# Kernel tuning notes

Measured on AMD Instinct MI355X. Metric: run time of the kernel, lower is better.

Reference implementation:

```python
import jax, jax.numpy as jnp
import numpy as np

N_MESS = 50000
MAX_NEI = 8
INPUT_SIZE = 128
H_SIZE = 128
DEPTH = 5


def setup_inputs() -> dict:
    key = jax.random.key(0)
    ks = jax.random.split(key, 7)
    s = 0.05
    fmess = jax.random.normal(ks[0], (N_MESS, INPUT_SIZE), dtype=jnp.float32)
    bgraph = jax.random.randint(ks[1], (N_MESS, MAX_NEI), 0, N_MESS, dtype=jnp.int32)
    # torch nn.Linear weights are [out_features, in_features]
    W_z = jax.random.normal(ks[2], (H_SIZE, INPUT_SIZE + H_SIZE), dtype=jnp.float32) * s
    b_z = jnp.zeros((H_SIZE,), jnp.float32)
    W_r = jax.random.normal(ks[3], (H_SIZE, INPUT_SIZE), dtype=jnp.float32) * s  # no bias
    U_r = jax.random.normal(ks[4], (H_SIZE, H_SIZE), dtype=jnp.float32) * s
    b_Ur = jnp.zeros((H_SIZE,), jnp.float32)
    W_h = jax.random.normal(ks[5], (H_SIZE, INPUT_SIZE + H_SIZE), dtype=jnp.float32) * s
    b_h = jnp.zeros((H_SIZE,), jnp.float32)
    return {"fmess": fmess, "bgraph": bgraph, "W_z": W_z, "b_z": b_z,
            "W_r": W_r, "U_r": U_r, "b_Ur": b_Ur, "W_h": W_h, "b_h": b_h}


def _gru_step(fmess, h_nei, W_z, b_z, W_r, U_r, b_Ur, W_h, b_h):
    # h_nei: [N, K, H]
    sum_h = h_nei.sum(axis=1)                                     # [N, H]
    z = jax.nn.sigmoid(jnp.concatenate([fmess, sum_h], axis=1) @ W_z.T + b_z)
    r_1 = (fmess @ W_r.T)[:, None, :]                             # [N, 1, H]
    r_2 = jnp.einsum('nkh,gh->nkg', h_nei, U_r) + b_Ur            # [N, K, H]
    r = jax.nn.sigmoid(r_1 + r_2)
    sum_gated_h = (r * h_nei).sum(axis=1)                         # [N, H]
    pre_h = jnp.tanh(jnp.concatenate([fmess, sum_gated_h], axis=1) @ W_h.T + b_h)
    return (1.0 - z) * sum_h + z * pre_h


def reference(fmess, bgraph, W_z, b_z, W_r, U_r, b_Ur, W_h, b_h):
    n = fmess.shape[0]
    h = jnp.zeros((n, H_SIZE), dtype=fmess.dtype)
    mask = jnp.ones((n, 1), dtype=fmess.dtype).at[0, 0].set(0.0)  # message 0 is padding
    for _ in range(DEPTH):
        h_nei = h[bgraph]                                         # gather: [N, K, H]
        h = _gru_step(fmess, h_nei, W_z, b_z, W_r, U_r, b_Ur, W_h, b_h)
        h = h * mask
    return h
```

## Files before the change

### kernel.cpp

```cpp
#include <hip/hip_runtime.h>
#include <hip/hip_bf16.h>

#define NM 50000
#define HD 128
#define KNEI 8
#define BM 64
#define SPAD 136
#define NBLK ((NM + BM - 1) / BM)
#define NH ((size_t)NM * (size_t)HD)

typedef float  fx4   __attribute__((ext_vector_type(4)));
typedef short  s16x8 __attribute__((ext_vector_type(8)));
typedef short  s16x4 __attribute__((ext_vector_type(4)));

__device__ __forceinline__ float sigm_f(float x) {
    return __builtin_amdgcn_rcpf(1.0f + __expf(-x));
}
__device__ __forceinline__ float tanh_f(float x) {
    return 2.0f * sigm_f(2.0f * x) - 1.0f;
}
__device__ __forceinline__ unsigned short f2b(float f) {
    __hip_bfloat16 h = __float2bfloat16(f);
    return __builtin_bit_cast(unsigned short, h);
}
__device__ __forceinline__ float b2f(unsigned short u) {
    __hip_bfloat16 h = __builtin_bit_cast(__hip_bfloat16, u);
    return __bfloat162float(h);
}

#define MFMA16(a, b, c) __builtin_amdgcn_mfma_f32_16x16x32_bf16(a, b, c, 0, 0, 0)

__device__ __forceinline__ void load_bfrag(const unsigned short* __restrict__ W,
                                           int ldw, int woff, int nf0, int l,
                                           s16x8 (&bf)[2][4])
{
    #pragma unroll
    for (int j = 0; j < 2; ++j) {
        const unsigned short* p =
            W + (size_t)((nf0 + j) * 16 + (l & 15)) * ldw + woff + ((l >> 4) << 3);
        #pragma unroll
        for (int ks = 0; ks < 4; ++ks)
            bf[j][ks] = *(const s16x8*)(p + ks * 32);
    }
}

__device__ __forceinline__ void pass(const unsigned short (*As)[SPAD],
                                     const s16x8 (&bf)[2][4],
                                     int l, fx4 (&acc)[4][2])
{
    const int kq = (l >> 4) << 3;
    #pragma unroll
    for (int ks = 0; ks < 4; ++ks)
        #pragma unroll
        for (int rb = 0; rb < 4; ++rb) {
            const s16x8 a = *(const s16x8*)&As[rb * 16 + (l & 15)][ks * 32 + kq];
            acc[rb][0] = MFMA16(a, bf[0][ks], acc[rb][0]);
            acc[rb][1] = MFMA16(a, bf[1][ks], acc[rb][1]);
        }
}

#define ZACC2(acc) { _Pragma("unroll") for (int z_ = 0; z_ < 4; ++z_) { \
                     acc[z_][0] = (fx4)0.0f; acc[z_][1] = (fx4)0.0f; } }

__device__ __forceinline__ void stage_A32(const float* __restrict__ A, int row0,
                                          unsigned short (*As)[SPAD], int tid)
{
    const int r  = tid & 63;
    const int c0 = (tid >> 6) << 5;
    int gr = row0 + r; if (gr >= NM) gr = NM - 1;
    const float* ap = A + (size_t)gr * HD + c0;
    #pragma unroll
    for (int j = 0; j < 32; j += 8) {
        s16x8 s;
        #pragma unroll
        for (int q = 0; q < 8; ++q) s[q] = (short)f2b(ap[j + q]);
        *(s16x8*)&As[r][c0 + j] = s;
    }
}

__device__ __forceinline__ void stage_A16(const unsigned short* __restrict__ A16, int row0,
                                          unsigned short (*As)[SPAD], int tid)
{
    const int r  = tid & 63;
    const int c0 = (tid >> 6) << 5;
    int gr = row0 + r; if (gr >= NM) gr = NM - 1;
    const unsigned short* ap = A16 + (size_t)gr * HD + c0;
    #pragma unroll
    for (int j = 0; j < 32; j += 8)
        *(s16x8*)&As[r][c0 + j] = *(const s16x8*)(ap + j);
}

__device__ __forceinline__ void lds_to_g16(const unsigned short (*L)[SPAD], int row0,
                                           unsigned short* __restrict__ G, int tid)
{
    const int r  = tid & 63;
    const int c0 = (tid >> 6) << 5;
    const int gr = row0 + r;
    if (gr >= NM) return;
    #pragma unroll
    for (int j = 0; j < 32; j += 8)
        *(s16x8*)&G[(size_t)gr * HD + c0 + j] = *(const s16x8*)&L[r][c0 + j];
}

__global__ __launch_bounds__(256)
void dgru_wcvt(const float* __restrict__ Wz, const float* __restrict__ Wr,
               const float* __restrict__ Ur, const float* __restrict__ Wh,
               unsigned short* __restrict__ w16)
{
    const int i = blockIdx.x * 256 + threadIdx.x;
    float v;
    if      (i < 32768) v = Wz[i];
    else if (i < 49152) v = Wr[i - 32768];
    else if (i < 65536) v = Ur[i - 49152];
    else                v = Wh[i - 65536];
    w16[i] = f2b(v);
}

__global__ __launch_bounds__(256, 3)
void dgru_pre(const float* __restrict__ fmess,
              const unsigned short* __restrict__ wz16,
              const unsigned short* __restrict__ wr16,
              const unsigned short* __restrict__ wh16,
              const unsigned short* __restrict__ ur16,
              const float* __restrict__ bz, const float* __restrict__ bh,
              const float* __restrict__ bur,
              unsigned short* __restrict__ fmess16,
              unsigned short* __restrict__ pre_r16,
              unsigned short* __restrict__ h16, unsigned short* __restrict__ uh16)
{
    __shared__ unsigned short AsF[BM][SPAD];
    __shared__ unsigned short AsX[BM][SPAD];
    const int tid  = threadIdx.x;
    const int row0 = blockIdx.x * BM;
    const int l    = tid & 63;
    const int nf0  = (tid >> 6) << 1;
    const int col0 = nf0 * 16 + (l & 15);
    const int rq   = (l >> 4) << 2;

    s16x8 bfA[2][4], bfB[2][4];
    load_bfrag(wz16, 2 * HD, 0, nf0, l, bfA);
    load_bfrag(wr16, HD, 0, nf0, l, bfB);
    stage_A32(fmess, row0, AsF, tid);
    __syncthreads();

    lds_to_g16(AsF, row0, fmess16, tid);

    fx4 zacc[4][2]; ZACC2(zacc);
    pass(AsF, bfA, l, zacc);
    load_bfrag(wh16, 2 * HD, 0, nf0, l, bfA);
    {
        fx4 racc[4][2]; ZACC2(racc);
        pass(AsF, bfB, l, racc);
        #pragma unroll
        for (int rb = 0; rb < 4; ++rb)
            #pragma unroll
            for (int j = 0; j < 2; ++j)
                #pragma unroll
                for (int q = 0; q < 4; ++q)
                    AsX[rb * 16 + rq + q][col0 + j * 16] = f2b(racc[rb][j][q]);
    }
    __syncthreads();
    lds_to_g16(AsX, row0, pre_r16, tid);

    fx4 hacc[4][2]; ZACC2(hacc);
    pass(AsF, bfA, l, hacc);
    load_bfrag(ur16, HD, 0, nf0, l, bfB);
    #pragma unroll
    for (int rb = 0; rb < 4; ++rb)
        #pragma unroll
        for (int j = 0; j < 2; ++j) {
            const float bvz = bz[col0 + j * 16];
            const float bvh = bh[col0 + j * 16];
            #pragma unroll
            for (int q = 0; q < 4; ++q) {
                const int gr = row0 + rb * 16 + rq + q;
                float h0 = sigm_f(zacc[rb][j][q] + bvz) * tanh_f(hacc[rb][j][q] + bvh);
                if (gr == 0) h0 = 0.0f;
                hacc[rb][j][q] = h0;
            }
        }
    __syncthreads();
    #pragma unroll
    for (int rb = 0; rb < 4; ++rb)
        #pragma unroll
        for (int j = 0; j < 2; ++j)
            #pragma unroll
            for (int q = 0; q < 4; ++q)
                AsX[rb * 16 + rq + q][col0 + j * 16] = f2b(hacc[rb][j][q]);
    __syncthreads();
    lds_to_g16(AsX, row0, h16, tid);
    {
        fx4 uacc[4][2]; ZACC2(uacc);
        pass(AsX, bfB, l, uacc);
        #pragma unroll
        for (int rb = 0; rb < 4; ++rb)
            #pragma unroll
            for (int j = 0; j < 2; ++j) {
                const float bv = bur[col0 + j * 16];
                #pragma unroll
                for (int q = 0; q < 4; ++q)
                    AsF[rb * 16 + rq + q][col0 + j * 16] = f2b(uacc[rb][j][q] + bv);
            }
    }
    __syncthreads();
    lds_to_g16(AsF, row0, uh16, tid);
}

__global__ __launch_bounds__(256)
void dgru_gather(const unsigned short* __restrict__ h16,
                 const unsigned short* __restrict__ uh16,
                 const int* __restrict__ bgraph,
                 const unsigned short* __restrict__ pre_r16,
                 unsigned short* __restrict__ sh16, unsigned short* __restrict__ sg16)
{
    const int tid = threadIdx.x;
    const int n   = blockIdx.x * 8 + (tid >> 5);
    const int d0  = (tid & 31) << 2;

    const int4* bg = (const int4*)(bgraph + (size_t)n * KNEI);
    const int4 b0 = bg[0], b1 = bg[1];
    const int idx[KNEI] = {b0.x, b0.y, b0.z, b0.w, b1.x, b1.y, b1.z, b1.w};

    s16x4 hr[KNEI], ur[KNEI];
    #pragma unroll
    for (int k = 0; k < KNEI; ++k)
        hr[k] = *(const s16x4*)&h16[(size_t)idx[k] * HD + d0];
    #pragma unroll
    for (int k = 0; k < KNEI; ++k)
        ur[k] = *(const s16x4*)&uh16[(size_t)idx[k] * HD + d0];
    const s16x4 prb = *(const s16x4*)&pre_r16[(size_t)n * HD + d0];
    float pr[4];
    #pragma unroll
    for (int j = 0; j < 4; ++j) pr[j] = b2f((unsigned short)prb[j]);

    float sh[4] = {0.f, 0.f, 0.f, 0.f};
    float sg[4] = {0.f, 0.f, 0.f, 0.f};
    #pragma unroll
    for (int k = 0; k < KNEI; ++k) {
        #pragma unroll
        for (int j = 0; j < 4; ++j) {
            const float hv = b2f((unsigned short)hr[k][j]);
            const float uv = b2f((unsigned short)ur[k][j]);
            sh[j] += hv;
            sg[j] = fmaf(sigm_f(pr[j] + uv), hv, sg[j]);
        }
    }
    s16x4 osh, osg;
    #pragma unroll
    for (int j = 0; j < 4; ++j) {
        osh[j] = (short)f2b(sh[j]);
        osg[j] = (short)f2b(sg[j]);
    }
    const size_t o = (size_t)n * HD + d0;
    *(s16x4*)&sh16[o] = osh;
    *(s16x4*)&sg16[o] = osg;
}

__global__ __launch_bounds__(256, 3)
void dgru_zh(const unsigned short* __restrict__ fmess16,
             const unsigned short* __restrict__ sh16,
             const unsigned short* __restrict__ sg16,
             const unsigned short* __restrict__ wz16,
             const unsigned short* __restrict__ wh16,
             const unsigned short* __restrict__ ur16,
             const float* __restrict__ bz, const float* __restrict__ bh,
             const float* __restrict__ bur,
             unsigned short* __restrict__ h16, unsigned short* __restrict__ uh16,
             float* __restrict__ hout, int last)
{
    __shared__ unsigned short AsF[BM][SPAD];
    __shared__ unsigned short AsX[BM][SPAD];
    const int tid  = threadIdx.x;
    const int row0 = blockIdx.x * BM;
    const int l    = tid & 63;
    const int nf0  = (tid >> 6) << 1;
    const int col0 = nf0 * 16 + (l & 15);
    const int rq   = (l >> 4) << 2;

    s16x8 bfA[2][4], bfB[2][4];
    load_bfrag(wz16, 2 * HD, 0,  nf0, l, bfA);
    load_bfrag(wz16, 2 * HD, HD, nf0, l, bfB);
    stage_A16(fmess16, row0, AsF, tid);
    stage_A16(sh16,    row0, AsX, tid);
    __syncthreads();

    fx4 zacc[4][2]; ZACC2(zacc);
    pass(AsF, bfA, l, zacc);
    pass(AsX, bfB, l, zacc);
    s16x4 shp[4][2];
    #pragma unroll
    for (int rb = 0; rb < 4; ++rb)
        #pragma unroll
        for (int j = 0; j < 2; ++j) {
            const float bv = bz[col0 + j * 16];
            #pragma unroll
            for (int q = 0; q < 4; ++q) {
                shp[rb][j][q] = (short)AsX[rb * 16 + rq + q][col0 + j * 16];
                zacc[rb][j][q] = sigm_f(zacc[rb][j][q] + bv);
            }
        }
    load_bfrag(wh16, 2 * HD, 0,  nf0, l, bfA);
    load_bfrag(wh16, 2 * HD, HD, nf0, l, bfB);
    __syncthreads();
    stage_A16(sg16, row0, AsX, tid);
    __syncthreads();

    fx4 hacc[4][2]; ZACC2(hacc);
    pass(AsF, bfA, l, hacc);
    pass(AsX, bfB, l, hacc);
    #pragma unroll
    for (int rb = 0; rb < 4; ++rb)
        #pragma unroll
        for (int j = 0; j < 2; ++j) {
            const float bv = bh[col0 + j * 16];
            #pragma unroll
            for (int q = 0; q < 4; ++q) {
                const int gr = row0 + rb * 16 + rq + q;
                const float zz = zacc[rb][j][q];
                const float sv = b2f((unsigned short)shp[rb][j][q]);
                float o = (1.0f - zz) * sv + zz * tanh_f(hacc[rb][j][q] + bv);
                if (gr == 0) o = 0.0f;
                hacc[rb][j][q] = o;
            }
        }
    if (last) {
        #pragma unroll
        for (int rb = 0; rb < 4; ++rb)
            #pragma unroll
            for (int j = 0; j < 2; ++j)
                #pragma unroll
                for (int q = 0; q < 4; ++q) {
                    const int gr = row0 + rb * 16 + rq + q;
                    if (gr < NM) hout[(size_t)gr * HD + col0 + j * 16] = hacc[rb][j][q];
                }
        return;
    }
    load_bfrag(ur16, HD, 0, nf0, l, bfA);
    __syncthreads();
    #pragma unroll
    for (int rb = 0; rb < 4; ++rb)
        #pragma unroll
        for (int j = 0; j < 2; ++j)
            #pragma unroll
            for (int q = 0; q < 4; ++q)
                AsF[rb * 16 + rq + q][col0 + j * 16] = f2b(hacc[rb][j][q]);
    __syncthreads();
    lds_to_g16(AsF, row0, h16, tid);
    {
        fx4 uacc[4][2]; ZACC2(uacc);
        pass(AsF, bfA, l, uacc);
        #pragma unroll
        for (int rb = 0; rb < 4; ++rb)
            #pragma unroll
            for (int j = 0; j < 2; ++j) {
                const float bv = bur[col0 + j * 16];
                #pragma unroll
                for (int q = 0; q < 4; ++q)
                    AsX[rb * 16 + rq + q][col0 + j * 16] = f2b(uacc[rb][j][q] + bv);
            }
    }
    __syncthreads();
    lds_to_g16(AsX, row0, uh16, tid);
}

extern "C" void kernel_launch(void* const* d_in, const int* in_sizes, int n_in,
                              void* d_out, int out_size, void* d_ws, size_t ws_size,
                              hipStream_t stream) {
    const float* fmess  = (const float*)d_in[0];
    const int*   bgraph = (const int*)  d_in[1];
    const float* W_z    = (const float*)d_in[2];
    const float* b_z    = (const float*)d_in[3];
    const float* W_r    = (const float*)d_in[4];
    const float* U_r    = (const float*)d_in[5];
    const float* b_Ur   = (const float*)d_in[6];
    const float* W_h    = (const float*)d_in[7];
    const float* b_h    = (const float*)d_in[8];

    unsigned short* ws16 = (unsigned short*)d_ws;
    unsigned short* fmess16 = ws16;
    unsigned short* pre_r16 = ws16 + NH;
    unsigned short* h16     = ws16 + 2 * NH;
    unsigned short* uh16    = ws16 + 3 * NH;
    unsigned short* sh16    = ws16 + 4 * NH;
    unsigned short* sg16    = ws16 + 5 * NH;
    unsigned short* w16     = ws16 + 6 * NH;
    unsigned short* wz16 = w16;
    unsigned short* wr16 = w16 + 32768;
    unsigned short* ur16 = w16 + 49152;
    unsigned short* wh16 = w16 + 65536;
    float* hout = (float*)d_out;

    dgru_wcvt<<<dim3(384), dim3(256), 0, stream>>>(W_z, W_r, U_r, W_h, w16);

    dgru_pre<<<dim3(NBLK), dim3(256), 0, stream>>>(
        fmess, wz16, wr16, wh16, ur16, b_z, b_h, b_Ur,
        fmess16, pre_r16, h16, uh16);

    for (int it = 1; it < 5; ++it) {
        dgru_gather<<<dim3(NM / 8), dim3(256), 0, stream>>>(
            h16, uh16, bgraph, pre_r16, sh16, sg16);
        dgru_zh<<<dim3(NBLK), dim3(256), 0, stream>>>(
            fmess16, sh16, sg16, wz16, wh16, ur16, b_z, b_h, b_Ur,
            h16, uh16, hout, (it == 4) ? 1 : 0);
    }
}
```

Before: 336.4 us.

## Fuse neighbor gather into GRU matmul kernel with ping-pong h buffers

Merges the separate gather kernel into the z/h GEMM kernel, so neighbor sums (sum_h and the gated sum) are built directly in shared memory rather than written to and reread from global memory. Because a block now reads neighbor rows that other blocks are updating, h and U_r·h are double-buffered across iterations. Blocks grow to 512 threads, one wave per 16-column slice, which halves the B-fragment registers per wave. This removes four kernel launches and the sh/sg round trips, at the cost of more per-block gather latency sitting in front of the MFMA work.

```diff
diff --git a/kernel.cpp b/kernel.cpp
--- a/kernel.cpp
+++ b/kernel.cpp
@@ -30,6 +30,29 @@
 
 #define MFMA16(a, b, c) __builtin_amdgcn_mfma_f32_16x16x32_bf16(a, b, c, 0, 0, 0)
 
+__device__ __forceinline__ void ldb1(const unsigned short* __restrict__ W,
+                                     int ldw, int woff, int w, int l, s16x8 (&bf)[4])
+{
+    const unsigned short* p =
+        W + (size_t)(w * 16 + (l & 15)) * ldw + woff + ((l >> 4) << 3);
+    #pragma unroll
+    for (int ks = 0; ks < 4; ++ks)
+        bf[ks] = *(const s16x8*)(p + ks * 32);
+}
+
+__device__ __forceinline__ void pass1(const unsigned short (*As)[SPAD],
+                                      const s16x8 (&bf)[4], int l, fx4 (&acc)[4])
+{
+    const int kq = (l >> 4) << 3;
+    #pragma unroll
+    for (int ks = 0; ks < 4; ++ks)
+        #pragma unroll
+        for (int rb = 0; rb < 4; ++rb) {
+            const s16x8 a = *(const s16x8*)&As[rb * 16 + (l & 15)][ks * 32 + kq];
+            acc[rb] = MFMA16(a, bf[ks], acc[rb]);
+        }
+}
+
 __device__ __forceinline__ void load_bfrag(const unsigned short* __restrict__ W,
                                            int ldw, int woff, int nf0, int l,
                                            s16x8 (&bf)[2][4])
@@ -78,18 +101,6 @@
     }
 }
 
-__device__ __forceinline__ void stage_A16(const unsigned short* __restrict__ A16, int row0,
-                                          unsigned short (*As)[SPAD], int tid)
-{
-    const int r  = tid & 63;
-    const int c0 = (tid >> 6) << 5;
-    int gr = row0 + r; if (gr >= NM) gr = NM - 1;
-    const unsigned short* ap = A16 + (size_t)gr * HD + c0;
-    #pragma unroll
-    for (int j = 0; j < 32; j += 8)
-        *(s16x8*)&As[r][c0 + j] = *(const s16x8*)(ap + j);
-}
-
 __device__ __forceinline__ void lds_to_g16(const unsigned short (*L)[SPAD], int row0,
                                            unsigned short* __restrict__ G, int tid)
 {
@@ -100,6 +111,28 @@
     #pragma unroll
     for (int j = 0; j < 32; j += 8)
         *(s16x8*)&G[(size_t)gr * HD + c0 + j] = *(const s16x8*)&L[r][c0 + j];
+}
+
+__device__ __forceinline__ void stage_A16_512(const unsigned short* __restrict__ A16,
+                                              int row0, unsigned short (*As)[SPAD], int tid)
+{
+    const int r  = tid & 63;
+    const int c0 = (tid >> 6) << 4;
+    int gr = row0 + r; if (gr >= NM) gr = NM - 1;
+    const unsigned short* ap = A16 + (size_t)gr * HD + c0;
+    *(s16x8*)&As[r][c0]     = *(const s16x8*)ap;
+    *(s16x8*)&As[r][c0 + 8] = *(const s16x8*)(ap + 8);
+}
+
+__device__ __forceinline__ void lds_to_g16_512(const unsigned short (*L)[SPAD], int row0,
+                                               unsigned short* __restrict__ G, int tid)
+{
+    const int r  = tid & 63;
+    const int c0 = (tid >> 6) << 4;
+    const int gr = row0 + r;
+    if (gr >= NM) return;
+    *(s16x8*)&G[(size_t)gr * HD + c0]     = *(const s16x8*)&L[r][c0];
+    *(s16x8*)&G[(size_t)gr * HD + c0 + 8] = *(const s16x8*)&L[r][c0 + 8];
 }
 
 __global__ __launch_bounds__(256)
@@ -206,161 +239,165 @@
     lds_to_g16(AsF, row0, uh16, tid);
 }
 
-__global__ __launch_bounds__(256)
-void dgru_gather(const unsigned short* __restrict__ h16,
-                 const unsigned short* __restrict__ uh16,
-                 const int* __restrict__ bgraph,
-                 const unsigned short* __restrict__ pre_r16,
-                 unsigned short* __restrict__ sh16, unsigned short* __restrict__ sg16)
-{
-    const int tid = threadIdx.x;
-    const int n   = blockIdx.x * 8 + (tid >> 5);
-    const int d0  = (tid & 31) << 2;
-
-    const int4* bg = (const int4*)(bgraph + (size_t)n * KNEI);
-    const int4 b0 = bg[0], b1 = bg[1];
-    const int idx[KNEI] = {b0.x, b0.y, b0.z, b0.w, b1.x, b1.y, b1.z, b1.w};
-
-    s16x4 hr[KNEI], ur[KNEI];
-    #pragma unroll
-    for (int k = 0; k < KNEI; ++k)
-        hr[k] = *(const s16x4*)&h16[(size_t)idx[k] * HD + d0];
-    #pragma unroll
-    for (int k = 0; k < KNEI; ++k)
-        ur[k] = *(const s16x4*)&uh16[(size_t)idx[k] * HD + d0];
-    const s16x4 prb = *(const s16x4*)&pre_r16[(size_t)n * HD + d0];
-    float pr[4];
-    #pragma unroll
-    for (int j = 0; j < 4; ++j) pr[j] = b2f((unsigned short)prb[j]);
-
-    float sh[4] = {0.f, 0.f, 0.f, 0.f};
-    float sg[4] = {0.f, 0.f, 0.f, 0.f};
-    #pragma unroll
-    for (int k = 0; k < KNEI; ++k) {
-        #pragma unroll
-        for (int j = 0; j < 4; ++j) {
-            const float hv = b2f((unsigned short)hr[k][j]);
-            const float uv = b2f((unsigned short)ur[k][j]);
-            sh[j] += hv;
-            sg[j] = fmaf(sigm_f(pr[j] + uv), hv, sg[j]);
-        }
-    }
-    s16x4 osh, osg;
-    #pragma unroll
-    for (int j = 0; j < 4; ++j) {
-        osh[j] = (short)f2b(sh[j]);
-        osg[j] = (short)f2b(sg[j]);
-    }
-    const size_t o = (size_t)n * HD + d0;
-    *(s16x4*)&sh16[o] = osh;
-    *(s16x4*)&sg16[o] = osg;
-}
-
-__global__ __launch_bounds__(256, 3)
-void dgru_zh(const unsigned short* __restrict__ fmess16,
-             const unsigned short* __restrict__ sh16,
-             const unsigned short* __restrict__ sg16,
-             const unsigned short* __restrict__ wz16,
-             const unsigned short* __restrict__ wh16,
-             const unsigned short* __restrict__ ur16,
-             const float* __restrict__ bz, const float* __restrict__ bh,
-             const float* __restrict__ bur,
-             unsigned short* __restrict__ h16, unsigned short* __restrict__ uh16,
-             float* __restrict__ hout, int last)
+__global__ __launch_bounds__(512, 4)
+void dgru_iter(const int* __restrict__ bgraph,
+               const unsigned short* __restrict__ pre_r16,
+               const unsigned short* __restrict__ fmess16,
+               const unsigned short* __restrict__ wz16,
+               const unsigned short* __restrict__ wh16,
+               const unsigned short* __restrict__ ur16,
+               const float* __restrict__ bz, const float* __restrict__ bh,
+               const float* __restrict__ bur,
+               const unsigned short* __restrict__ h16r,
+               const unsigned short* __restrict__ uh16r,
+               unsigned short* __restrict__ h16w,
+               unsigned short* __restrict__ uh16w,
+               float* __restrict__ hout, int last)
 {
     __shared__ unsigned short AsF[BM][SPAD];
-    __shared__ unsigned short AsX[BM][SPAD];
+    __shared__ unsigned short AsH[BM][SPAD];
+    __shared__ unsigned short AsG[BM][SPAD];
     const int tid  = threadIdx.x;
     const int row0 = blockIdx.x * BM;
+    const int w    = tid >> 6;
     const int l    = tid & 63;
-    const int nf0  = (tid >> 6) << 1;
-    const int col0 = nf0 * 16 + (l & 15);
+    const int col0 = w * 16 + (l & 15);
     const int rq   = (l >> 4) << 2;
 
-    s16x8 bfA[2][4], bfB[2][4];
-    load_bfrag(wz16, 2 * HD, 0,  nf0, l, bfA);
-    load_bfrag(wz16, 2 * HD, HD, nf0, l, bfB);
-    stage_A16(fmess16, row0, AsF, tid);
-    stage_A16(sh16,    row0, AsX, tid);
-    __syncthreads();
-
-    fx4 zacc[4][2]; ZACC2(zacc);
-    pass(AsF, bfA, l, zacc);
-    pass(AsX, bfB, l, zacc);
-    s16x4 shp[4][2];
-    #pragma unroll
-    for (int rb = 0; rb < 4; ++rb)
-        #pragma unroll
-        for (int j = 0; j < 2; ++j) {
-            const float bv = bz[col0 + j * 16];
+    {
+        const int m  = tid >> 3;
+        const int d0 = (tid & 7) << 4;
+        int n = row0 + m; if (n >= NM) n = NM - 1;
+
+        const int4* bg = (const int4*)(bgraph + (size_t)n * KNEI);
+        const int4 bA = bg[0], bB = bg[1];
+        const int idx[KNEI] = {bA.x, bA.y, bA.z, bA.w, bB.x, bB.y, bB.z, bB.w};
+
+        float pr[16];
+        {
+            const unsigned short* p = pre_r16 + (size_t)n * HD + d0;
+            const s16x8 a = *(const s16x8*)p;
+            const s16x8 b = *(const s16x8*)(p + 8);
+            #pragma unroll
+            for (int j = 0; j < 8; ++j) {
+                pr[j]     = b2f((unsigned short)a[j]);
+                pr[8 + j] = b2f((unsigned short)b[j]);
+            }
+        }
+        float sh[16], sg[16];
+        #pragma unroll
+        for (int j = 0; j < 16; ++j) { sh[j] = 0.0f; sg[j] = 0.0f; }
+
+        #pragma unroll
+        for (int k = 0; k < KNEI; ++k) {
+            const unsigned short* hp = h16r  + (size_t)idx[k] * HD + d0;
+            const unsigned short* up = uh16r + (size_t)idx[k] * HD + d0;
+            const s16x8 h0 = *(const s16x8*)hp, h1 = *(const s16x8*)(hp + 8);
+            const s16x8 u0 = *(const s16x8*)up, u1 = *(const s16x8*)(up + 8);
+            #pragma unroll
+            for (int j = 0; j < 8; ++j) {
+                const float hv = b2f((unsigned short)h0[j]);
+                const float uv = b2f((unsigned short)u0[j]);
+                sh[j] += hv;
+                sg[j] = fmaf(sigm_f(pr[j] + uv), hv, sg[j]);
+            }
+            #pragma unroll
+            for (int j = 0; j < 8; ++j) {
+                const float hv = b2f((unsigned short)h1[j]);
+                const float uv = b2f((unsigned short)u1[j]);
+                sh[8 + j] += hv;
+                sg[8 + j] = fmaf(sigm_f(pr[8 + j] + uv), hv, sg[8 + j]);
+            }
+        }
+        s16x8 o0, o1, g0, g1;
+        #pragma unroll
+        for (int j = 0; j < 8; ++j) {
+            o0[j] = (short)f2b(sh[j]);     o1[j] = (short)f2b(sh[8 + j]);
+            g0[j] = (short)f2b(sg[j]);     g1[j] = (short)f2b(sg[8 + j]);
+        }
+        *(s16x8*)&AsH[m][d0]     = o0;
+        *(s16x8*)&AsH[m][d0 + 8] = o1;
+        *(s16x8*)&AsG[m][d0]     = g0;
+        *(s16x8*)&AsG[m][d0 + 8] = g1;
+    }
+    stage_A16_512(fmess16, row0, AsF, tid);
+    __syncthreads();
+
+    s16x8 bfA[4], bfB[4];
+    ldb1(wz16, 2 * HD, 0,  w, l, bfA);
+    ldb1(wz16, 2 * HD, HD, w, l, bfB);
+    fx4 zacc[4];
+    #pragma unroll
+    for (int rb = 0; rb < 4; ++rb) zacc[rb] = (fx4)0.0f;
+    pass1(AsF, bfA, l, zacc);
+    pass1(AsH, bfB, l, zacc);
+    float shv[4][4];
+    {
+        const float bv = bz[col0];
+        #pragma unroll
+        for (int rb = 0; rb < 4; ++rb)
             #pragma unroll
             for (int q = 0; q < 4; ++q) {
-                shp[rb][j][q] = (short)AsX[rb * 16 + rq + q][col0 + j * 16];
-                zacc[rb][j][q] = sigm_f(zacc[rb][j][q] + bv);
-            }
-        }
-    load_bfrag(wh16, 2 * HD, 0,  nf0, l, bfA);
-    load_bfrag(wh16, 2 * HD, HD, nf0, l, bfB);
-    __syncthreads();
-    stage_A16(sg16, row0, AsX, tid);
-    __syncthreads();
-
-    fx4 hacc[4][2]; ZACC2(hacc);
-    pass(AsF, bfA, l, hacc);
-    pass(AsX, bfB, l, hacc);
-    #pragma unroll
-    for (int rb = 0; rb < 4; ++rb)
-        #pragma unroll
-        for (int j = 0; j < 2; ++j) {
-            const float bv = bh[col0 + j * 16];
+                shv[rb][q] = b2f(AsH[rb * 16 + rq + q][col0]);
+                zacc[rb][q] = sigm_f(zacc[rb][q] + bv);
+            }
+    }
+
+    ldb1(wh16, 2 * HD, 0,  w, l, bfA);
+    ldb1(wh16, 2 * HD, HD, w, l, bfB);
+    fx4 hacc[4];
+    #pragma unroll
+    for (int rb = 0; rb < 4; ++rb) hacc[rb] = (fx4)0.0f;
+    pass1(AsF, bfA, l, hacc);
+    pass1(AsG, bfB, l, hacc);
+    {
+        const float bv = bh[col0];
+        #pragma unroll
+        for (int rb = 0; rb < 4; ++rb)
             #pragma unroll
             for (int q = 0; q < 4; ++q) {
                 const int gr = row0 + rb * 16 + rq + q;
-                const float zz = zacc[rb][j][q];
-                const float sv = b2f((unsigned short)shp[rb][j][q]);
-                float o = (1.0f - zz) * sv + zz * tanh_f(hacc[rb][j][q] + bv);
+                const float zz = zacc[rb][q];
+                float o = (1.0f - zz) * shv[rb][q] + zz * tanh_f(hacc[rb][q] + bv);
                 if (gr == 0) o = 0.0f;
-                hacc[rb][j][q] = o;
-            }
-        }
+                hacc[rb][q] = o;
+            }
+    }
     if (last) {
         #pragma unroll
         for (int rb = 0; rb < 4; ++rb)
             #pragma unroll
-            for (int j = 0; j < 2; ++j)
-                #pragma unroll
-                for (int q = 0; q < 4; ++q) {
-                    const int gr = row0 + rb * 16 + rq + q;
-                    if (gr < NM) hout[(size_t)gr * HD + col0 + j * 16] = hacc[rb][j][q];
-                }
+            for (int q = 0; q < 4; ++q) {
+                const int gr = row0 + rb * 16 + rq + q;
+                if (gr < NM) hout[(size_t)gr * HD + col0] = hacc[rb][q];
+            }
         return;
     }
-    load_bfrag(ur16, HD, 0, nf0, l, bfA);
+
+    ldb1(ur16, HD, 0, w, l, bfA);
     __syncthreads();
     #pragma unroll
     for (int rb = 0; rb < 4; ++rb)
         #pragma unroll
-        for (int j = 0; j < 2; ++j)
+        for (int q = 0; q < 4; ++q)
+            AsF[rb * 16 + rq + q][col0] = f2b(hacc[rb][q]);
+    __syncthreads();
+    lds_to_g16_512(AsF, row0, h16w, tid);
+
+    fx4 uacc[4];
+    #pragma unroll
+    for (int rb = 0; rb < 4; ++rb) uacc[rb] = (fx4)0.0f;
+    pass1(AsF, bfA, l, uacc);
+    {
+        const float bv = bur[col0];
+        #pragma unroll
+        for (int rb = 0; rb < 4; ++rb)
             #pragma unroll
             for (int q = 0; q < 4; ++q)
-                AsF[rb * 16 + rq + q][col0 + j * 16] = f2b(hacc[rb][j][q]);
-    __syncthreads();
-    lds_to_g16(AsF, row0, h16, tid);
-    {
-        fx4 uacc[4][2]; ZACC2(uacc);
-        pass(AsF, bfA, l, uacc);
-        #pragma unroll
-        for (int rb = 0; rb < 4; ++rb)
-            #pragma unroll
-            for (int j = 0; j < 2; ++j) {
-                const float bv = bur[col0 + j * 16];
-                #pragma unroll
-                for (int q = 0; q < 4; ++q)
-                    AsX[rb * 16 + rq + q][col0 + j * 16] = f2b(uacc[rb][j][q] + bv);
-            }
-    }
-    __syncthreads();
-    lds_to_g16(AsX, row0, uh16, tid);
+                AsH[rb * 16 + rq + q][col0] = f2b(uacc[rb][q] + bv);
+    }
+    __syncthreads();
+    lds_to_g16_512(AsH, row0, uh16w, tid);
 }
 
 extern "C" void kernel_launch(void* const* d_in, const int* in_sizes, int n_in,
@@ -379,10 +416,10 @@
     unsigned short* ws16 = (unsigned short*)d_ws;
     unsigned short* fmess16 = ws16;
     unsigned short* pre_r16 = ws16 + NH;
-    unsigned short* h16     = ws16 + 2 * NH;
-    unsigned short* uh16    = ws16 + 3 * NH;
-    unsigned short* sh16    = ws16 + 4 * NH;
-    unsigned short* sg16    = ws16 + 5 * NH;
+    unsigned short* h16a    = ws16 + 2 * NH;
+    unsigned short* uh16a   = ws16 + 3 * NH;
+    unsigned short* h16b    = ws16 + 4 * NH;
+    unsigned short* uh16b   = ws16 + 5 * NH;
     unsigned short* w16     = ws16 + 6 * NH;
     unsigned short* wz16 = w16;
     unsigned short* wr16 = w16 + 32768;
@@ -394,13 +431,16 @@
 
     dgru_pre<<<dim3(NBLK), dim3(256), 0, stream>>>(
         fmess, wz16, wr16, wh16, ur16, b_z, b_h, b_Ur,
-        fmess16, pre_r16, h16, uh16);
+        fmess16, pre_r16, h16a, uh16a);
 
     for (int it = 1; it < 5; ++it) {
-        dgru_gather<<<dim3(NM / 8), dim3(256), 0, stream>>>(
-            h16, uh16, bgraph, pre_r16, sh16, sg16);
-        dgru_zh<<<dim3(NBLK), dim3(256), 0, stream>>>(
-            fmess16, sh16, sg16, wz16, wh16, ur16, b_z, b_h, b_Ur,
-            h16, uh16, hout, (it == 4) ? 1 : 0);
-    }
-}
+        const int pa = (it & 1);
+        const unsigned short* hr = pa ? h16a : h16b;
+        const unsigned short* ur = pa ? uh16a : uh16b;
+        unsigned short* hw = pa ? h16b : h16a;
+        unsigned short* uw = pa ? uh16b : uh16a;
+        dgru_iter<<<dim3(NBLK), dim3(512), 0, stream>>>(
+            bgraph, pre_r16, fmess16, wz16, wh16, ur16, b_z, b_h, b_Ur,
+            hr, ur, hw, uw, hout, (it == 4) ? 1 : 0);
+    }
+}
```

After: 482.9 us. 43.5% more time.

## Precompute loop-invariant fmess projections for z and h gates once

Applied to the files above, without the earlier changes.

The fmess @ W_z[:, :H] and fmess @ W_h[:, :H] products (plus biases) are the same in every GRU iteration, so dgru_pre now computes them once and stores them as bf16 in an MFMA-fragment-ordered layout. Each dgru_zh call reads them back per lane instead of restaging fmess and doing two extra GEMM passes. The z and h GEMMs now share one staging step with no intermediate sync. This removes half of the per-iteration MFMA work and one LDS restage, at the cost of storing the pre-activations in bf16, which adds some rounding.

```diff
diff --git a/kernel.cpp b/kernel.cpp
--- a/kernel.cpp
+++ b/kernel.cpp
@@ -8,6 +8,7 @@
 #define SPAD 136
 #define NBLK ((NM + BM - 1) / BM)
 #define NH ((size_t)NM * (size_t)HD)
+#define FRAG 8192
 
 typedef float  fx4   __attribute__((ext_vector_type(4)));
 typedef short  s16x8 __attribute__((ext_vector_type(8)));
@@ -61,6 +62,10 @@
 
 #define ZACC2(acc) { _Pragma("unroll") for (int z_ = 0; z_ < 4; ++z_) { \
                      acc[z_][0] = (fx4)0.0f; acc[z_][1] = (fx4)0.0f; } }
+
+__device__ __forceinline__ size_t faddr(int blk, int nf0, int j, int rb, int l) {
+    return (size_t)blk * FRAG + (size_t)((nf0 + j) * 4 + rb) * 256 + (size_t)l * 4;
+}
 
 __device__ __forceinline__ void stage_A32(const float* __restrict__ A, int row0,
                                           unsigned short (*As)[SPAD], int tid)
@@ -124,14 +129,16 @@
               const unsigned short* __restrict__ ur16,
               const float* __restrict__ bz, const float* __restrict__ bh,
               const float* __restrict__ bur,
-              unsigned short* __restrict__ fmess16,
+              unsigned short* __restrict__ pre_z16,
+              unsigned short* __restrict__ pre_hf16,
               unsigned short* __restrict__ pre_r16,
               unsigned short* __restrict__ h16, unsigned short* __restrict__ uh16)
 {
     __shared__ unsigned short AsF[BM][SPAD];
     __shared__ unsigned short AsX[BM][SPAD];
     const int tid  = threadIdx.x;
-    const int row0 = blockIdx.x * BM;
+    const int blk  = blockIdx.x;
+    const int row0 = blk * BM;
     const int l    = tid & 63;
     const int nf0  = (tid >> 6) << 1;
     const int col0 = nf0 * 16 + (l & 15);
@@ -142,8 +149,6 @@
     load_bfrag(wr16, HD, 0, nf0, l, bfB);
     stage_A32(fmess, row0, AsF, tid);
     __syncthreads();
-
-    lds_to_g16(AsF, row0, fmess16, tid);
 
     fx4 zacc[4][2]; ZACC2(zacc);
     pass(AsF, bfA, l, zacc);
@@ -171,13 +176,20 @@
         for (int j = 0; j < 2; ++j) {
             const float bvz = bz[col0 + j * 16];
             const float bvh = bh[col0 + j * 16];
+            s16x4 pz, ph;
             #pragma unroll
             for (int q = 0; q < 4; ++q) {
+                const float zlog = zacc[rb][j][q] + bvz;
+                const float hlog = hacc[rb][j][q] + bvh;
+                pz[q] = (short)f2b(zlog);
+                ph[q] = (short)f2b(hlog);
                 const int gr = row0 + rb * 16 + rq + q;
-                float h0 = sigm_f(zacc[rb][j][q] + bvz) * tanh_f(hacc[rb][j][q] + bvh);
+                float h0 = sigm_f(zlog) * tanh_f(hlog);
                 if (gr == 0) h0 = 0.0f;
                 hacc[rb][j][q] = h0;
             }
+            *(s16x4*)&pre_z16[faddr(blk, nf0, j, rb, l)]  = pz;
+            *(s16x4*)&pre_hf16[faddr(blk, nf0, j, rb, l)] = ph;
         }
     __syncthreads();
     #pragma unroll
@@ -257,68 +269,52 @@
 }
 
 __global__ __launch_bounds__(256, 3)
-void dgru_zh(const unsigned short* __restrict__ fmess16,
+void dgru_zh(const unsigned short* __restrict__ pre_z16,
+             const unsigned short* __restrict__ pre_hf16,
              const unsigned short* __restrict__ sh16,
              const unsigned short* __restrict__ sg16,
              const unsigned short* __restrict__ wz16,
              const unsigned short* __restrict__ wh16,
              const unsigned short* __restrict__ ur16,
-             const float* __restrict__ bz, const float* __restrict__ bh,
              const float* __restrict__ bur,
              unsigned short* __restrict__ h16, unsigned short* __restrict__ uh16,
              float* __restrict__ hout, int last)
 {
-    __shared__ unsigned short AsF[BM][SPAD];
+    __shared__ unsigned short AsH[BM][SPAD];
     __shared__ unsigned short AsX[BM][SPAD];
     const int tid  = threadIdx.x;
-    const int row0 = blockIdx.x * BM;
+    const int blk  = blockIdx.x;
+    const int row0 = blk * BM;
     const int l    = tid & 63;
     const int nf0  = (tid >> 6) << 1;
     const int col0 = nf0 * 16 + (l & 15);
     const int rq   = (l >> 4) << 2;
 
     s16x8 bfA[2][4], bfB[2][4];
-    load_bfrag(wz16, 2 * HD, 0,  nf0, l, bfA);
-    load_bfrag(wz16, 2 * HD, HD, nf0, l, bfB);
-    stage_A16(fmess16, row0, AsF, tid);
-    stage_A16(sh16,    row0, AsX, tid);
+    load_bfrag(wz16, 2 * HD, HD, nf0, l, bfA);
+    load_bfrag(wh16, 2 * HD, HD, nf0, l, bfB);
+    stage_A16(sh16, row0, AsH, tid);
+    stage_A16(sg16, row0, AsX, tid);
     __syncthreads();
 
     fx4 zacc[4][2]; ZACC2(zacc);
-    pass(AsF, bfA, l, zacc);
-    pass(AsX, bfB, l, zacc);
-    s16x4 shp[4][2];
+    pass(AsH, bfA, l, zacc);
+    fx4 hacc[4][2]; ZACC2(hacc);
+    pass(AsX, bfB, l, hacc);
+    load_bfrag(ur16, HD, 0, nf0, l, bfA);
     #pragma unroll
     for (int rb = 0; rb < 4; ++rb)
         #pragma unroll
         for (int j = 0; j < 2; ++j) {
-            const float bv = bz[col0 + j * 16];
-            #pragma unroll
-            for (int q = 0; q < 4; ++q) {
-                shp[rb][j][q] = (short)AsX[rb * 16 + rq + q][col0 + j * 16];
-                zacc[rb][j][q] = sigm_f(zacc[rb][j][q] + bv);
-            }
-        }
-    load_bfrag(wh16, 2 * HD, 0,  nf0, l, bfA);
-    load_bfrag(wh16, 2 * HD, HD, nf0, l, bfB);
-    __syncthreads();
-    stage_A16(sg16, row0, AsX, tid);
-    __syncthreads();
-
-    fx4 hacc[4][2]; ZACC2(hacc);
-    pass(AsF, bfA, l, hacc);
-    pass(AsX, bfB, l, hacc);
-    #pragma unroll
-    for (int rb = 0; rb < 4; ++rb)
-        #pragma unroll
-        for (int j = 0; j < 2; ++j) {
-            const float bv = bh[col0 + j * 16];
+            const s16x4 pz = *(const s16x4*)&pre_z16[faddr(blk, nf0, j, rb, l)];
+            const s16x4 ph = *(const s16x4*)&pre_hf16[faddr(blk, nf0, j, rb, l)];
             #pragma unroll
             for (int q = 0; q < 4; ++q) {
                 const int gr = row0 + rb * 16 + rq + q;
-                const float zz = zacc[rb][j][q];
-                const float sv = b2f((unsigned short)shp[rb][j][q]);
-                float o = (1.0f - zz) * sv + zz * tanh_f(hacc[rb][j][q] + bv);
+                const float zz = sigm_f(b2f((unsigned short)pz[q]) + zacc[rb][j][q]);
+                const float sv = b2f(AsH[rb * 16 + rq + q][col0 + j * 16]);
+                float o = (1.0f - zz) * sv
+                        + zz * tanh_f(b2f((unsigned short)ph[q]) + hacc[rb][j][q]);
                 if (gr == 0) o = 0.0f;
                 hacc[rb][j][q] = o;
             }
@@ -335,7 +331,6 @@
                 }
         return;
     }
-    load_bfrag(ur16, HD, 0, nf0, l, bfA);
     __syncthreads();
     #pragma unroll
     for (int rb = 0; rb < 4; ++rb)
@@ -343,12 +338,12 @@
         for (int j = 0; j < 2; ++j)
             #pragma unroll
             for (int q = 0; q < 4; ++q)
-                AsF[rb * 16 + rq + q][col0 + j * 16] = f2b(hacc[rb][j][q]);
-    __syncthreads();
-    lds_to_g16(AsF, row0, h16, tid);
+                AsH[rb * 16 + rq + q][col0 + j * 16] = f2b(hacc[rb][j][q]);
+    __syncthreads();
+    lds_to_g16(AsH, row0, h16, tid);
     {
         fx4 uacc[4][2]; ZACC2(uacc);
-        pass(AsF, bfA, l, uacc);
+        pass(AsH, bfA, l, uacc);
         #pragma unroll
         for (int rb = 0; rb < 4; ++rb)
             #pragma unroll
@@ -377,13 +372,15 @@
     const float* b_h    = (const float*)d_in[8];
 
     unsigned short* ws16 = (unsigned short*)d_ws;
-    unsigned short* fmess16 = ws16;
-    unsigned short* pre_r16 = ws16 + NH;
-    unsigned short* h16     = ws16 + 2 * NH;
-    unsigned short* uh16    = ws16 + 3 * NH;
-    unsigned short* sh16    = ws16 + 4 * NH;
-    unsigned short* sg16    = ws16 + 5 * NH;
-    unsigned short* w16     = ws16 + 6 * NH;
+    const size_t FPAD = (size_t)NBLK * FRAG;
+    unsigned short* pre_z16  = ws16;
+    unsigned short* pre_hf16 = ws16 + FPAD;
+    unsigned short* pre_r16  = ws16 + 2 * FPAD;
+    unsigned short* h16      = pre_r16 + NH;
+    unsigned short* uh16     = h16 + NH;
+    unsigned short* sh16     = uh16 + NH;
+    unsigned short* sg16     = sh16 + NH;
+    unsigned short* w16      = sg16 + NH;
     unsigned short* wz16 = w16;
     unsigned short* wr16 = w16 + 32768;
     unsigned short* ur16 = w16 + 49152;
@@ -394,13 +391,13 @@
 
     dgru_pre<<<dim3(NBLK), dim3(256), 0, stream>>>(
         fmess, wz16, wr16, wh16, ur16, b_z, b_h, b_Ur,
-        fmess16, pre_r16, h16, uh16);
+        pre_z16, pre_hf16, pre_r16, h16, uh16);
 
     for (int it = 1; it < 5; ++it) {
         dgru_gather<<<dim3(NM / 8), dim3(256), 0, stream>>>(
             h16, uh16, bgraph, pre_r16, sh16, sg16);
         dgru_zh<<<dim3(NBLK), dim3(256), 0, stream>>>(
-            fmess16, sh16, sg16, wz16, wh16, ur16, b_z, b_h, b_Ur,
+            pre_z16, pre_hf16, sh16, sg16, wz16, wh16, ur16, b_Ur,
             h16, uh16, hout, (it == 4) ? 1 : 0);
     }
 }
```

New measurement: 275.9 us (median of 2 runs). 1.22x faster.
